# Performance work log

Measured on AMD Instinct MI355X. Metric: run time of the kernel, lower is better.

Reference implementation:

```python
import jax, jax.numpy as jnp
import numpy as np

COMMITMENT_COST = 0.25  # hardcoded in VQVAEModel (quantizer commitment_cost=0.25)


def setup_inputs() -> dict:
    key = jax.random.key(0)
    k1, k2 = jax.random.split(key)
    B, D, H, W = 128, 64, 32, 32
    K = 512
    inputs = jax.random.normal(k1, (B, D, H, W), dtype=jnp.float32)
    codebook = jax.random.normal(k2, (K, D), dtype=jnp.float32)  # nn.Embedding weight, normal_()
    return {"inputs": inputs, "codebook": codebook}


def reference(inputs, codebook):
    # VectorQuantizerEMA.forward in eval mode (no EMA buffer update).
    B, D, H, W = inputs.shape
    K = codebook.shape[0]
    # BCHW -> BHWC
    x = jnp.transpose(inputs, (0, 2, 3, 1))
    flat = x.reshape(-1, D)  # [N, D], N = B*H*W
    distances = (jnp.sum(flat * flat, axis=1, keepdims=True)
                 + jnp.sum(codebook * codebook, axis=1)
                 - 2.0 * flat @ codebook.T)
    # max_one_hot(-distances) == one-hot of argmin(distances)
    idx = jnp.argmin(distances, axis=1)  # [N]
    oh = jax.nn.one_hot(idx, K, dtype=flat.dtype)  # [N, K]
    # quantized = onehot @ codebook (detached) == gather, same math, cheaper
    quantized = jax.lax.stop_gradient(codebook[idx]).reshape(x.shape)  # [B,H,W,D]
    # commitment loss (quantized is detached under torch.no_grad)
    e_latent_loss = jnp.mean((quantized - x) ** 2)
    loss = COMMITMENT_COST * e_latent_loss
    # straight-through estimator
    q_st = x + jax.lax.stop_gradient(quantized - x)
    # perplexity of codebook usage
    avg_probs = jnp.mean(oh, axis=0)
    perplexity = jnp.exp(-jnp.sum(avg_probs * jnp.log(avg_probs + 1e-10)))
    # oh_encodings: rearrange '(b n) d -> b d n'
    oh_encodings = jnp.transpose(oh.reshape(B, H * W, K), (0, 2, 1))  # [B, K, N]
    quantized_out = jnp.transpose(q_st, (0, 3, 1, 2))  # back to BCHW
    return loss, quantized_out, perplexity, oh_encodings
```

## Files before the change

### kernel.cpp

```cpp
#include <hip/hip_runtime.h>
#include <hip/hip_bf16.h>
#include <float.h>

#define NTOT 131072

#define OFF_LOSS  0
#define OFF_QUANT 1
#define OFF_PERP  8388609
#define OFF_OH    8388610

#define FLAG_BIT (1 << 16)
#define TAU      1.5e-3f
#define MAGIC    0x5EEDF00D
#define WSTRIDE  516

typedef __attribute__((ext_vector_type(8))) short short8;
typedef __attribute__((ext_vector_type(4))) short short4v;
typedef __attribute__((ext_vector_type(4))) float f32x4;

__device__ inline unsigned short f2bf(float f) {
    unsigned u = __builtin_bit_cast(unsigned, f);
    unsigned r = (u + 0x7fffu + ((u >> 16) & 1u)) >> 16;
    return (unsigned short)r;
}
__device__ inline float bf2f(unsigned short h) {
    return __builtin_bit_cast(float, ((unsigned)h) << 16);
}

__global__ __launch_bounds__(1024)
void vq_fused(const float* __restrict__ x, const float* __restrict__ cb,
              int* __restrict__ wsi, float* __restrict__ out) {
    __shared__ short Ehi[512 * 64];
    __shared__ short Elo[512 * 64];
    __shared__ float en_s[512];
    __shared__ float dist_s[512];
    __shared__ int   idx_s[512];
    __shared__ int   hist_s[512];

    const int t = threadIdx.x, wg = blockIdx.x;
    const int w = t >> 6, lane = t & 63;
    const int c = lane & 15, g = lane >> 4;
    const int b0 = wg >> 1;
    const int sphalf = (wg & 1) << 9;
    float* qout = out + OFF_QUANT;
    float* oh   = out + OFF_OH;

    if (t < 512) hist_s[t] = 0;

    const float4* cb4 = (const float4*)cb;
#pragma unroll
    for (int i = 0; i < 8; ++i) {
        int e4 = i * 1024 + t;
        float4 v = cb4[e4];
        int k = e4 >> 4, q = e4 & 15;
        int base = (k << 6) + ((((q >> 1) ^ (k & 7)) << 3) + ((q & 1) << 2));
        float vv[4] = {v.x, v.y, v.z, v.w};
        short4v h4, l4;
#pragma unroll
        for (int e = 0; e < 4; ++e) {
            unsigned short h = f2bf(vv[e]);
            h4[e] = (short)h;
            l4[e] = (short)f2bf(vv[e] - bf2f(h));
        }
        *(short4v*)&Ehi[base] = h4;
        *(short4v*)&Elo[base] = l4;
    }
    if (t < 512) {
        const float4* r4 = cb4 + (t << 4);
        float s = 0.f;
#pragma unroll
        for (int j = 0; j < 16; ++j) {
            float4 vv = r4[j];
            s = fmaf(vv.x, vv.x, s); s = fmaf(vv.y, vv.y, s);
            s = fmaf(vv.z, vv.z, s); s = fmaf(vv.w, vv.w, s);
        }
        en_s[t] = s;
    }

    short8 bh[2][2], bl[2][2];
    float xn2[2] = {0.f, 0.f};
    const float* xb = x + (((size_t)b0) << 16) + sphalf + (w << 5) + c;
#pragma unroll
    for (int xt = 0; xt < 2; ++xt) {
#pragma unroll
        for (int ks = 0; ks < 2; ++ks) {
            short8 h8, l8;
#pragma unroll
            for (int e = 0; e < 8; ++e) {
                float xv = xb[(xt << 4) + ((size_t)((ks << 5) + (g << 3) + e) << 10)];
                unsigned short hh = f2bf(xv);
                h8[e] = (short)hh;
                l8[e] = (short)f2bf(xv - bf2f(hh));
                xn2[xt] = fmaf(xv, xv, xn2[xt]);
            }
            bh[xt][ks] = h8; bl[xt][ks] = l8;
        }
    }
    float xnorm[2];
#pragma unroll
    for (int xt = 0; xt < 2; ++xt) {
        float v = xn2[xt];
        v += __shfl_xor(v, 16);
        v += __shfl_xor(v, 32);
        xnorm[xt] = v;
    }
    __syncthreads();

    float v1[2] = {FLT_MAX, FLT_MAX}, v2[2] = {FLT_MAX, FLT_MAX};
    int   i1[2] = {0, 0},            i2v[2] = {0, 0};
    const int sw = c & 7;
    const short* ph = &Ehi[c << 6];
    const short* pl = &Elo[c << 6];
#pragma unroll 2
    for (int kt = 0; kt < 32; ++kt) {
        const short* rh = ph + (kt << 10);
        const short* rl = pl + (kt << 10);
        short8 ah0 = *(const short8*)(rh + ((g ^ sw) << 3));
        short8 ah1 = *(const short8*)(rh + (((g + 4) ^ sw) << 3));
        short8 al0 = *(const short8*)(rl + ((g ^ sw) << 3));
        short8 al1 = *(const short8*)(rl + (((g + 4) ^ sw) << 3));
        float4 en4 = *(const float4*)&en_s[(kt << 4) + (g << 2)];
        float en_[4] = {en4.x, en4.y, en4.z, en4.w};
#pragma unroll
        for (int xt = 0; xt < 2; ++xt) {
            f32x4 acc = {0.f, 0.f, 0.f, 0.f};
            acc = __builtin_amdgcn_mfma_f32_16x16x32_bf16(ah0, bh[xt][0], acc, 0, 0, 0);
            acc = __builtin_amdgcn_mfma_f32_16x16x32_bf16(ah1, bh[xt][1], acc, 0, 0, 0);
            acc = __builtin_amdgcn_mfma_f32_16x16x32_bf16(al0, bh[xt][0], acc, 0, 0, 0);
            acc = __builtin_amdgcn_mfma_f32_16x16x32_bf16(al1, bh[xt][1], acc, 0, 0, 0);
            acc = __builtin_amdgcn_mfma_f32_16x16x32_bf16(ah0, bl[xt][0], acc, 0, 0, 0);
            acc = __builtin_amdgcn_mfma_f32_16x16x32_bf16(ah1, bl[xt][1], acc, 0, 0, 0);
#pragma unroll
            for (int r = 0; r < 4; ++r) {
                float dd = fmaf(-2.0f, acc[r], en_[r]);
                int k = (kt << 4) + (g << 2) + r;
                bool lt1 = dd < v1[xt];
                bool lt2 = dd < v2[xt];
                v2[xt] = lt1 ? v1[xt] : (lt2 ? dd : v2[xt]);
                i2v[xt] = lt1 ? i1[xt] : (lt2 ? k : i2v[xt]);
                v1[xt] = lt1 ? dd : v1[xt];
                i1[xt] = lt1 ? k : i1[xt];
            }
        }
    }

#pragma unroll
    for (int xt = 0; xt < 2; ++xt) {
        float V1 = v1[xt], V2 = v2[xt]; int I1 = i1[xt], I2 = i2v[xt];
#pragma unroll
        for (int off = 16; off <= 32; off <<= 1) {
            float o1 = __shfl_xor(V1, off); int oi1 = __shfl_xor(I1, off);
            float o2 = __shfl_xor(V2, off); int oi2 = __shfl_xor(I2, off);
            if (o1 < V1 || (o1 == V1 && oi1 < I1)) {
                V2 = V1; I2 = I1; V1 = o1; I1 = oi1;
            } else if (o1 < V2 || (o1 == V2 && oi1 < I2)) { V2 = o1; I2 = oi1; }
            if (o2 < V2 || (o2 == V2 && oi2 < I2)) { V2 = o2; I2 = oi2; }
        }
        if (g == 0) {
            int r = (w << 5) + (xt << 4) + c;
            idx_s[r]  = I1 | ((V2 - V1 < TAU) ? FLAG_BIT : 0);
            dist_s[r] = xnorm[xt] + V1;
        }
    }
    __syncthreads();

    {
        int rowfull = (lane < 32) ? idx_s[(w << 5) + lane] : 0;
        unsigned long long m = __ballot((lane < 32) && (rowfull & FLAG_BIT));
        while (m) {
            int r = __ffsll((long long)m) - 1; m &= m - 1;
            int sp = sphalf + (w << 5) + r;
            float xd = x[(((size_t)b0) << 16) + (((size_t)lane) << 10) + sp];
            double bestd = 1e300; int besti = 0x7fffffff;
            for (int kk = 0; kk < 8; ++kk) {
                int k = (lane << 3) + kk;
                double s = 0.0;
#pragma unroll
                for (int d4 = 0; d4 < 16; ++d4) {
                    float4 e4 = cb4[(k << 4) + d4];
                    float x0 = __shfl(xd, d4 * 4 + 0);
                    float x1 = __shfl(xd, d4 * 4 + 1);
                    float x2 = __shfl(xd, d4 * 4 + 2);
                    float x3 = __shfl(xd, d4 * 4 + 3);
                    double f0 = (double)x0 - (double)e4.x; s = fma(f0, f0, s);
                    double f1 = (double)x1 - (double)e4.y; s = fma(f1, f1, s);
                    double f2 = (double)x2 - (double)e4.z; s = fma(f2, f2, s);
                    double f3 = (double)x3 - (double)e4.w; s = fma(f3, f3, s);
                }
                if (s < bestd || (s == bestd && k < besti)) { bestd = s; besti = k; }
            }
#pragma unroll
            for (int off = 32; off; off >>= 1) {
                double od = __shfl_xor(bestd, off);
                int    oi = __shfl_xor(besti, off);
                if (od < bestd || (od == bestd && oi < besti)) { bestd = od; besti = oi; }
            }
            if (lane == 0) {
                idx_s[(w << 5) + r]  = besti;
                dist_s[(w << 5) + r] = (float)bestd;
            }
        }
    }
    __syncthreads();

    if (t < 512) {
        int k = idx_s[t] & 511;
        idx_s[t] = k;
        atomicAdd(&hist_s[k], 1);
        float v = dist_s[t];
#pragma unroll
        for (int off = 1; off < 64; off <<= 1) v += __shfl_xor(v, off);
        if (lane == 0) en_s[w] = v;
    }
    __syncthreads();
    if (t < 512)
        __hip_atomic_store(&wsi[wg * WSTRIDE + t], hist_s[t],
                           __ATOMIC_RELAXED, __HIP_MEMORY_SCOPE_AGENT);
    if (t == 0) {
        float lsum = 0.f;
        for (int i = 0; i < 8; ++i) lsum += en_s[i];
        __hip_atomic_store(&wsi[wg * WSTRIDE + 512], __float_as_int(lsum),
                           __ATOMIC_RELAXED, __HIP_MEMORY_SCOPE_AGENT);
    }
    __syncthreads();
    if (t == 0)
        __hip_atomic_store(&wsi[wg * WSTRIDE + 513], MAGIC,
                           __ATOMIC_RELEASE, __HIP_MEMORY_SCOPE_AGENT);

    {
        float4 z4 = {0.f, 0.f, 0.f, 0.f};
        float2 z2 = {0.f, 0.f};
        float* base_wg = oh + (((size_t)b0) << 19) + sphalf;
        for (int j = 0; j < 32; ++j) {
            int k = w + (j << 4);
            float* cbase = base_wg + (((size_t)k) << 10);
            *(float4*)(cbase + 2 + (lane << 2)) = z4;
            if (lane < 63)
                *(float4*)(cbase + 2 + ((64 + lane) << 2)) = z4;
            else {
                *(float2*)(cbase)       = z2;
                *(float2*)(cbase + 510) = z2;
            }
        }
    }
    __syncthreads();

    if (t < 512) {
        int k = idx_s[t];
        oh[(((size_t)b0) << 19) + (((size_t)k) << 10) + sphalf + t] = 1.0f;
    }

    {
        float* qbase = qout + (((size_t)b0) << 16) + sphalf;
#pragma unroll
        for (int j = 0; j < 4; ++j) {
            int d = (w << 2) + j;
            const int ch = d >> 3, dj = d & 7;
            float* rb = qbase + (((size_t)d) << 10);
#pragma unroll
            for (int rnd = 0; rnd < 2; ++rnd) {
                int m = (rnd << 6) + lane;
                if (m < 127) {
                    int s0 = 3 + (m << 2);
                    float vv[4];
#pragma unroll
                    for (int e = 0; e < 4; ++e) {
                        int k = idx_s[s0 + e];
                        int a = (k << 6) + (((ch ^ (k & 7)) << 3) + dj);
                        vv[e] = bf2f((unsigned short)Ehi[a]) + bf2f((unsigned short)Elo[a]);
                    }
                    float4 v4 = {vv[0], vv[1], vv[2], vv[3]};
                    *(float4*)(rb + s0) = v4;
                } else if (rnd == 1) {
                    int k0 = idx_s[0], k1 = idx_s[1], k2 = idx_s[2], k5 = idx_s[511];
                    int a0 = (k0 << 6) + (((ch ^ (k0 & 7)) << 3) + dj);
                    int a1 = (k1 << 6) + (((ch ^ (k1 & 7)) << 3) + dj);
                    int a2 = (k2 << 6) + (((ch ^ (k2 & 7)) << 3) + dj);
                    int a5 = (k5 << 6) + (((ch ^ (k5 & 7)) << 3) + dj);
                    rb[0] = bf2f((unsigned short)Ehi[a0]) + bf2f((unsigned short)Elo[a0]);
                    float2 e2 = { bf2f((unsigned short)Ehi[a1]) + bf2f((unsigned short)Elo[a1]),
                                  bf2f((unsigned short)Ehi[a2]) + bf2f((unsigned short)Elo[a2]) };
                    *(float2*)(rb + 1) = e2;
                    rb[511] = bf2f((unsigned short)Ehi[a5]) + bf2f((unsigned short)Elo[a5]);
                }
            }
        }
    }

    if (wg == 0) {
        if (t < 256) {
            while (__hip_atomic_load(&wsi[t * WSTRIDE + 513],
                                     __ATOMIC_ACQUIRE, __HIP_MEMORY_SCOPE_AGENT) != MAGIC)
                __builtin_amdgcn_s_sleep(2);
        }
        __syncthreads();
        float plog = 0.f, lpart = 0.f;
        if (t < 512) {
            int s = 0;
            for (int wgi = 0; wgi < 256; ++wgi)
                s += __hip_atomic_load(&wsi[wgi * WSTRIDE + t],
                                       __ATOMIC_RELAXED, __HIP_MEMORY_SCOPE_AGENT);
            float p = (float)s * (1.f / (float)NTOT);
            plog = p * logf(p + 1e-10f);
        }
        if (t < 256)
            lpart = __int_as_float(__hip_atomic_load(&wsi[t * WSTRIDE + 512],
                                       __ATOMIC_RELAXED, __HIP_MEMORY_SCOPE_AGENT));
#pragma unroll
        for (int off = 1; off < 64; off <<= 1) {
            plog  += __shfl_xor(plog, off);
            lpart += __shfl_xor(lpart, off);
        }
        __syncthreads();
        if (lane == 0 && w < 8) en_s[w] = plog;
        if (lane == 0 && w < 4) dist_s[w] = lpart;
        __syncthreads();
        if (t == 0) {
            float ps = 0.f; for (int i = 0; i < 8; ++i) ps += en_s[i];
            float ls = 0.f; for (int i = 0; i < 4; ++i) ls += dist_s[i];
            out[OFF_PERP] = expf(-ps);
            out[OFF_LOSS] = 0.25f * ls / ((float)NTOT * 64.0f);
        }
    }
}

extern "C" void kernel_launch(void* const* d_in, const int* in_sizes, int n_in,
                              void* d_out, int out_size, void* d_ws, size_t ws_size,
                              hipStream_t stream) {
    const float* x  = (const float*)d_in[0];
    const float* cb = (const float*)d_in[1];
    vq_fused<<<256, 1024, 0, stream>>>(x, cb, (int*)d_ws, (float*)d_out);
}
```

Measured before the change: 417.6 us.

## Specialize waves: half compute argmin while other half zero one-hot output

Splits the 16 waves into two roles. Eight waves load inputs and run the MFMA distance/argmin over 64 rows each. The other eight waves convert the codebook into LDS during setup, then write the large zero fill of the one-hot output while the compute waves run. This hides the memory-bound zeroing behind the MFMA work and drops one barrier. In exchange, the compute waves carry twice the rows, so register pressure rises, and the codebook staging now runs on half the threads.

```diff
diff --git a/kernel.cpp b/kernel.cpp
--- a/kernel.cpp
+++ b/kernel.cpp
@@ -48,156 +48,176 @@
     if (t < 512) hist_s[t] = 0;
 
     const float4* cb4 = (const float4*)cb;
-#pragma unroll
-    for (int i = 0; i < 8; ++i) {
-        int e4 = i * 1024 + t;
-        float4 v = cb4[e4];
-        int k = e4 >> 4, q = e4 & 15;
-        int base = (k << 6) + ((((q >> 1) ^ (k & 7)) << 3) + ((q & 1) << 2));
-        float vv[4] = {v.x, v.y, v.z, v.w};
-        short4v h4, l4;
-#pragma unroll
-        for (int e = 0; e < 4; ++e) {
-            unsigned short h = f2bf(vv[e]);
-            h4[e] = (short)h;
-            l4[e] = (short)f2bf(vv[e] - bf2f(h));
-        }
-        *(short4v*)&Ehi[base] = h4;
-        *(short4v*)&Elo[base] = l4;
-    }
-    if (t < 512) {
-        const float4* r4 = cb4 + (t << 4);
-        float s = 0.f;
-#pragma unroll
-        for (int j = 0; j < 16; ++j) {
-            float4 vv = r4[j];
-            s = fmaf(vv.x, vv.x, s); s = fmaf(vv.y, vv.y, s);
-            s = fmaf(vv.z, vv.z, s); s = fmaf(vv.w, vv.w, s);
-        }
-        en_s[t] = s;
-    }
-
-    short8 bh[2][2], bl[2][2];
-    float xn2[2] = {0.f, 0.f};
-    const float* xb = x + (((size_t)b0) << 16) + sphalf + (w << 5) + c;
-#pragma unroll
-    for (int xt = 0; xt < 2; ++xt) {
-#pragma unroll
-        for (int ks = 0; ks < 2; ++ks) {
-            short8 h8, l8;
-#pragma unroll
-            for (int e = 0; e < 8; ++e) {
-                float xv = xb[(xt << 4) + ((size_t)((ks << 5) + (g << 3) + e) << 10)];
-                unsigned short hh = f2bf(xv);
-                h8[e] = (short)hh;
-                l8[e] = (short)f2bf(xv - bf2f(hh));
-                xn2[xt] = fmaf(xv, xv, xn2[xt]);
-            }
-            bh[xt][ks] = h8; bl[xt][ks] = l8;
-        }
-    }
-    float xnorm[2];
-#pragma unroll
-    for (int xt = 0; xt < 2; ++xt) {
-        float v = xn2[xt];
-        v += __shfl_xor(v, 16);
-        v += __shfl_xor(v, 32);
-        xnorm[xt] = v;
+
+    short8 bh[4][2], bl[4][2];
+    float xnorm[4];
+
+    if (w >= 8) {
+        int j = w - 8;
+#pragma unroll
+        for (int i = 0; i < 16; ++i) {
+            int e4 = (j << 6) + lane + (i << 9);
+            float4 v = cb4[e4];
+            int k = e4 >> 4, q = e4 & 15;
+            int base = (k << 6) + ((((q >> 1) ^ (k & 7)) << 3) + ((q & 1) << 2));
+            float vv[4] = {v.x, v.y, v.z, v.w};
+            short4v h4, l4;
+#pragma unroll
+            for (int e = 0; e < 4; ++e) {
+                unsigned short h = f2bf(vv[e]);
+                h4[e] = (short)h;
+                l4[e] = (short)f2bf(vv[e] - bf2f(h));
+            }
+            *(short4v*)&Ehi[base] = h4;
+            *(short4v*)&Elo[base] = l4;
+        }
+        {
+            int i = t - 512;
+            const float4* r4 = cb4 + (i << 4);
+            float s = 0.f;
+#pragma unroll
+            for (int jj = 0; jj < 16; ++jj) {
+                float4 vv = r4[jj];
+                s = fmaf(vv.x, vv.x, s); s = fmaf(vv.y, vv.y, s);
+                s = fmaf(vv.z, vv.z, s); s = fmaf(vv.w, vv.w, s);
+            }
+            en_s[i] = s;
+        }
+    } else {
+        const float* xb = x + (((size_t)b0) << 16) + sphalf + (w << 6) + c;
+#pragma unroll
+        for (int xt = 0; xt < 4; ++xt) {
+            float xn2 = 0.f;
+#pragma unroll
+            for (int ks = 0; ks < 2; ++ks) {
+                short8 h8, l8;
+#pragma unroll
+                for (int e = 0; e < 8; ++e) {
+                    float xv = xb[(xt << 4) + ((size_t)((ks << 5) + (g << 3) + e) << 10)];
+                    unsigned short hh = f2bf(xv);
+                    h8[e] = (short)hh;
+                    l8[e] = (short)f2bf(xv - bf2f(hh));
+                    xn2 = fmaf(xv, xv, xn2);
+                }
+                bh[xt][ks] = h8; bl[xt][ks] = l8;
+            }
+            xn2 += __shfl_xor(xn2, 16);
+            xn2 += __shfl_xor(xn2, 32);
+            xnorm[xt] = xn2;
+        }
     }
     __syncthreads();
 
-    float v1[2] = {FLT_MAX, FLT_MAX}, v2[2] = {FLT_MAX, FLT_MAX};
-    int   i1[2] = {0, 0},            i2v[2] = {0, 0};
-    const int sw = c & 7;
-    const short* ph = &Ehi[c << 6];
-    const short* pl = &Elo[c << 6];
-#pragma unroll 2
-    for (int kt = 0; kt < 32; ++kt) {
-        const short* rh = ph + (kt << 10);
-        const short* rl = pl + (kt << 10);
-        short8 ah0 = *(const short8*)(rh + ((g ^ sw) << 3));
-        short8 ah1 = *(const short8*)(rh + (((g + 4) ^ sw) << 3));
-        short8 al0 = *(const short8*)(rl + ((g ^ sw) << 3));
-        short8 al1 = *(const short8*)(rl + (((g + 4) ^ sw) << 3));
-        float4 en4 = *(const float4*)&en_s[(kt << 4) + (g << 2)];
-        float en_[4] = {en4.x, en4.y, en4.z, en4.w};
-#pragma unroll
-        for (int xt = 0; xt < 2; ++xt) {
-            f32x4 acc = {0.f, 0.f, 0.f, 0.f};
-            acc = __builtin_amdgcn_mfma_f32_16x16x32_bf16(ah0, bh[xt][0], acc, 0, 0, 0);
-            acc = __builtin_amdgcn_mfma_f32_16x16x32_bf16(ah1, bh[xt][1], acc, 0, 0, 0);
-            acc = __builtin_amdgcn_mfma_f32_16x16x32_bf16(al0, bh[xt][0], acc, 0, 0, 0);
-            acc = __builtin_amdgcn_mfma_f32_16x16x32_bf16(al1, bh[xt][1], acc, 0, 0, 0);
-            acc = __builtin_amdgcn_mfma_f32_16x16x32_bf16(ah0, bl[xt][0], acc, 0, 0, 0);
-            acc = __builtin_amdgcn_mfma_f32_16x16x32_bf16(ah1, bl[xt][1], acc, 0, 0, 0);
-#pragma unroll
-            for (int r = 0; r < 4; ++r) {
-                float dd = fmaf(-2.0f, acc[r], en_[r]);
-                int k = (kt << 4) + (g << 2) + r;
-                bool lt1 = dd < v1[xt];
-                bool lt2 = dd < v2[xt];
-                v2[xt] = lt1 ? v1[xt] : (lt2 ? dd : v2[xt]);
-                i2v[xt] = lt1 ? i1[xt] : (lt2 ? k : i2v[xt]);
-                v1[xt] = lt1 ? dd : v1[xt];
-                i1[xt] = lt1 ? k : i1[xt];
-            }
-        }
-    }
-
-#pragma unroll
-    for (int xt = 0; xt < 2; ++xt) {
-        float V1 = v1[xt], V2 = v2[xt]; int I1 = i1[xt], I2 = i2v[xt];
-#pragma unroll
-        for (int off = 16; off <= 32; off <<= 1) {
-            float o1 = __shfl_xor(V1, off); int oi1 = __shfl_xor(I1, off);
-            float o2 = __shfl_xor(V2, off); int oi2 = __shfl_xor(I2, off);
-            if (o1 < V1 || (o1 == V1 && oi1 < I1)) {
-                V2 = V1; I2 = I1; V1 = o1; I1 = oi1;
-            } else if (o1 < V2 || (o1 == V2 && oi1 < I2)) { V2 = o1; I2 = oi1; }
-            if (o2 < V2 || (o2 == V2 && oi2 < I2)) { V2 = o2; I2 = oi2; }
-        }
-        if (g == 0) {
-            int r = (w << 5) + (xt << 4) + c;
-            idx_s[r]  = I1 | ((V2 - V1 < TAU) ? FLAG_BIT : 0);
-            dist_s[r] = xnorm[xt] + V1;
-        }
-    }
-    __syncthreads();
-
-    {
-        int rowfull = (lane < 32) ? idx_s[(w << 5) + lane] : 0;
-        unsigned long long m = __ballot((lane < 32) && (rowfull & FLAG_BIT));
-        while (m) {
-            int r = __ffsll((long long)m) - 1; m &= m - 1;
-            int sp = sphalf + (w << 5) + r;
-            float xd = x[(((size_t)b0) << 16) + (((size_t)lane) << 10) + sp];
-            double bestd = 1e300; int besti = 0x7fffffff;
-            for (int kk = 0; kk < 8; ++kk) {
-                int k = (lane << 3) + kk;
-                double s = 0.0;
-#pragma unroll
-                for (int d4 = 0; d4 < 16; ++d4) {
-                    float4 e4 = cb4[(k << 4) + d4];
-                    float x0 = __shfl(xd, d4 * 4 + 0);
-                    float x1 = __shfl(xd, d4 * 4 + 1);
-                    float x2 = __shfl(xd, d4 * 4 + 2);
-                    float x3 = __shfl(xd, d4 * 4 + 3);
-                    double f0 = (double)x0 - (double)e4.x; s = fma(f0, f0, s);
-                    double f1 = (double)x1 - (double)e4.y; s = fma(f1, f1, s);
-                    double f2 = (double)x2 - (double)e4.z; s = fma(f2, f2, s);
-                    double f3 = (double)x3 - (double)e4.w; s = fma(f3, f3, s);
-                }
-                if (s < bestd || (s == bestd && k < besti)) { bestd = s; besti = k; }
-            }
-#pragma unroll
-            for (int off = 32; off; off >>= 1) {
-                double od = __shfl_xor(bestd, off);
-                int    oi = __shfl_xor(besti, off);
-                if (od < bestd || (od == bestd && oi < besti)) { bestd = od; besti = oi; }
-            }
-            if (lane == 0) {
-                idx_s[(w << 5) + r]  = besti;
-                dist_s[(w << 5) + r] = (float)bestd;
+    if (w < 8) {
+        float v1[4] = {FLT_MAX, FLT_MAX, FLT_MAX, FLT_MAX};
+        float v2[4] = {FLT_MAX, FLT_MAX, FLT_MAX, FLT_MAX};
+        int   i1[4] = {0, 0, 0, 0}, i2v[4] = {0, 0, 0, 0};
+        const int sw = c & 7;
+        const short* ph = &Ehi[c << 6];
+        const short* pl = &Elo[c << 6];
+        for (int kt = 0; kt < 32; ++kt) {
+            const short* rh = ph + (kt << 10);
+            const short* rl = pl + (kt << 10);
+            short8 ah0 = *(const short8*)(rh + ((g ^ sw) << 3));
+            short8 ah1 = *(const short8*)(rh + (((g + 4) ^ sw) << 3));
+            short8 al0 = *(const short8*)(rl + ((g ^ sw) << 3));
+            short8 al1 = *(const short8*)(rl + (((g + 4) ^ sw) << 3));
+            float4 en4 = *(const float4*)&en_s[(kt << 4) + (g << 2)];
+            float en_[4] = {en4.x, en4.y, en4.z, en4.w};
+#pragma unroll
+            for (int xt = 0; xt < 4; ++xt) {
+                f32x4 acc = {0.f, 0.f, 0.f, 0.f};
+                acc = __builtin_amdgcn_mfma_f32_16x16x32_bf16(ah0, bh[xt][0], acc, 0, 0, 0);
+                acc = __builtin_amdgcn_mfma_f32_16x16x32_bf16(ah1, bh[xt][1], acc, 0, 0, 0);
+                acc = __builtin_amdgcn_mfma_f32_16x16x32_bf16(al0, bh[xt][0], acc, 0, 0, 0);
+                acc = __builtin_amdgcn_mfma_f32_16x16x32_bf16(al1, bh[xt][1], acc, 0, 0, 0);
+                acc = __builtin_amdgcn_mfma_f32_16x16x32_bf16(ah0, bl[xt][0], acc, 0, 0, 0);
+                acc = __builtin_amdgcn_mfma_f32_16x16x32_bf16(ah1, bl[xt][1], acc, 0, 0, 0);
+#pragma unroll
+                for (int r = 0; r < 4; ++r) {
+                    float dd = fmaf(-2.0f, acc[r], en_[r]);
+                    int k = (kt << 4) + (g << 2) + r;
+                    bool lt1 = dd < v1[xt];
+                    bool lt2 = dd < v2[xt];
+                    v2[xt] = lt1 ? v1[xt] : (lt2 ? dd : v2[xt]);
+                    i2v[xt] = lt1 ? i1[xt] : (lt2 ? k : i2v[xt]);
+                    v1[xt] = lt1 ? dd : v1[xt];
+                    i1[xt] = lt1 ? k : i1[xt];
+                }
+            }
+        }
+
+#pragma unroll
+        for (int xt = 0; xt < 4; ++xt) {
+            float V1 = v1[xt], V2 = v2[xt]; int I1 = i1[xt], I2 = i2v[xt];
+#pragma unroll
+            for (int off = 16; off <= 32; off <<= 1) {
+                float o1 = __shfl_xor(V1, off); int oi1 = __shfl_xor(I1, off);
+                float o2 = __shfl_xor(V2, off); int oi2 = __shfl_xor(I2, off);
+                if (o1 < V1 || (o1 == V1 && oi1 < I1)) {
+                    V2 = V1; I2 = I1; V1 = o1; I1 = oi1;
+                } else if (o1 < V2 || (o1 == V2 && oi1 < I2)) { V2 = o1; I2 = oi1; }
+                if (o2 < V2 || (o2 == V2 && oi2 < I2)) { V2 = o2; I2 = oi2; }
+            }
+            if (g == 0) {
+                int r = (w << 6) + (xt << 4) + c;
+                idx_s[r]  = I1 | ((V2 - V1 < TAU) ? FLAG_BIT : 0);
+                dist_s[r] = xnorm[xt] + V1;
+            }
+        }
+
+        for (int half = 0; half < 2; ++half) {
+            int rbase = (w << 6) + (half << 5);
+            int rowfull = (lane < 32) ? idx_s[rbase + lane] : 0;
+            unsigned long long m = __ballot((lane < 32) && (rowfull & FLAG_BIT));
+            while (m) {
+                int r = __ffsll((long long)m) - 1; m &= m - 1;
+                int sp = sphalf + rbase + r;
+                float xd = x[(((size_t)b0) << 16) + (((size_t)lane) << 10) + sp];
+                double bestd = 1e300; int besti = 0x7fffffff;
+                for (int kk = 0; kk < 8; ++kk) {
+                    int k = (lane << 3) + kk;
+                    double s = 0.0;
+#pragma unroll
+                    for (int d4 = 0; d4 < 16; ++d4) {
+                        float4 e4 = cb4[(k << 4) + d4];
+                        float x0 = __shfl(xd, d4 * 4 + 0);
+                        float x1 = __shfl(xd, d4 * 4 + 1);
+                        float x2 = __shfl(xd, d4 * 4 + 2);
+                        float x3 = __shfl(xd, d4 * 4 + 3);
+                        double f0 = (double)x0 - (double)e4.x; s = fma(f0, f0, s);
+                        double f1 = (double)x1 - (double)e4.y; s = fma(f1, f1, s);
+                        double f2 = (double)x2 - (double)e4.z; s = fma(f2, f2, s);
+                        double f3 = (double)x3 - (double)e4.w; s = fma(f3, f3, s);
+                    }
+                    if (s < bestd || (s == bestd && k < besti)) { bestd = s; besti = k; }
+                }
+#pragma unroll
+                for (int off = 32; off; off >>= 1) {
+                    double od = __shfl_xor(bestd, off);
+                    int    oi = __shfl_xor(besti, off);
+                    if (od < bestd || (od == bestd && oi < besti)) { bestd = od; besti = oi; }
+                }
+                if (lane == 0) {
+                    idx_s[rbase + r]  = besti;
+                    dist_s[rbase + r] = (float)bestd;
+                }
+            }
+        }
+    } else {
+        int j = w - 8;
+        float4 z4 = {0.f, 0.f, 0.f, 0.f};
+        float2 z2 = {0.f, 0.f};
+        float* base_wg = oh + (((size_t)b0) << 19) + sphalf;
+        for (int it = 0; it < 64; ++it) {
+            int k = j + (it << 3);
+            float* cbase = base_wg + (((size_t)k) << 10);
+            *(float4*)(cbase + 2 + (lane << 2)) = z4;
+            if (lane < 63)
+                *(float4*)(cbase + 2 + ((64 + lane) << 2)) = z4;
+            else {
+                *(float2*)(cbase)       = z2;
+                *(float2*)(cbase + 510) = z2;
             }
         }
     }
@@ -226,24 +246,6 @@
     if (t == 0)
         __hip_atomic_store(&wsi[wg * WSTRIDE + 513], MAGIC,
                            __ATOMIC_RELEASE, __HIP_MEMORY_SCOPE_AGENT);
-
-    {
-        float4 z4 = {0.f, 0.f, 0.f, 0.f};
-        float2 z2 = {0.f, 0.f};
-        float* base_wg = oh + (((size_t)b0) << 19) + sphalf;
-        for (int j = 0; j < 32; ++j) {
-            int k = w + (j << 4);
-            float* cbase = base_wg + (((size_t)k) << 10);
-            *(float4*)(cbase + 2 + (lane << 2)) = z4;
-            if (lane < 63)
-                *(float4*)(cbase + 2 + ((64 + lane) << 2)) = z4;
-            else {
-                *(float2*)(cbase)       = z2;
-                *(float2*)(cbase + 510) = z2;
-            }
-        }
-    }
-    __syncthreads();
 
     if (t < 512) {
         int k = idx_s[t];
```

After: 413.2 us. About the same (-1.1%).

## Split codebook prep kernel, halve block size and LDS, use global atomics for stats

Applied to the files above, without the earlier changes.

Adds a small prep kernel that precomputes the bf16 low-part codebook into workspace and zeroes the global counters. The main kernel now runs 512 blocks of 512 threads, keeps only the high part in LDS and reads the low part from global/L2. The per-block histogram/loss handoff through a polled workspace array is replaced by global atomicAdds and a done counter. The quantized output is gathered straight from the fp32 codebook. The smaller LDS footprint is meant to raise occupancy, at the cost of an extra launch and global-memory loads in the inner MFMA loop.

```diff
diff --git a/kernel.cpp b/kernel.cpp
--- a/kernel.cpp
+++ b/kernel.cpp
@@ -11,8 +11,8 @@
 
 #define FLAG_BIT (1 << 16)
 #define TAU      1.5e-3f
-#define MAGIC    0x5EEDF00D
-#define WSTRIDE  516
+
+#define W_ELO 640
 
 typedef __attribute__((ext_vector_type(8))) short short8;
 typedef __attribute__((ext_vector_type(4))) short short4v;
@@ -27,45 +27,65 @@
     return __builtin_bit_cast(float, ((unsigned)h) << 16);
 }
 
-__global__ __launch_bounds__(1024)
-void vq_fused(const float* __restrict__ x, const float* __restrict__ cb,
-              int* __restrict__ wsi, float* __restrict__ out) {
+__global__ __launch_bounds__(512)
+void vq_prep(const float* __restrict__ cb, int* __restrict__ wsi) {
+    int tid = blockIdx.x * 512 + threadIdx.x;
+    if (tid < 514) wsi[tid] = 0;
+    short* elo = (short*)(wsi + W_ELO);
+    int row = tid >> 1, half = tid & 1;
+    const float4* cb4 = (const float4*)cb;
+#pragma unroll
+    for (int j = 0; j < 8; ++j) {
+        float4 v = cb4[(row << 4) + (half << 3) + j];
+        float vv[4] = {v.x, v.y, v.z, v.w};
+        short4v l4;
+#pragma unroll
+        for (int e = 0; e < 4; ++e) {
+            unsigned short h = f2bf(vv[e]);
+            l4[e] = (short)f2bf(vv[e] - bf2f(h));
+        }
+        *(short4v*)(elo + (row << 6) + (half << 5) + (j << 2)) = l4;
+    }
+}
+
+__global__ __launch_bounds__(512, 4)
+void vq_main(const float* __restrict__ x, const float* __restrict__ cb,
+             int* __restrict__ wsi, float* __restrict__ out) {
     __shared__ short Ehi[512 * 64];
-    __shared__ short Elo[512 * 64];
     __shared__ float en_s[512];
-    __shared__ float dist_s[512];
-    __shared__ int   idx_s[512];
+    __shared__ float dist_s[256];
+    __shared__ int   idx_s[256];
     __shared__ int   hist_s[512];
+    __shared__ float lpart_s[4];
 
     const int t = threadIdx.x, wg = blockIdx.x;
     const int w = t >> 6, lane = t & 63;
     const int c = lane & 15, g = lane >> 4;
-    const int b0 = wg >> 1;
-    const int sphalf = (wg & 1) << 9;
+    const int b = wg >> 2;
+    const int sp0 = (wg & 3) << 8;
     float* qout = out + OFF_QUANT;
     float* oh   = out + OFF_OH;
+    float* loss_g = (float*)wsi;
+    int*   done_g = wsi + 1;
+    int*   cnt_g  = wsi + 2;
+    const short* elo_t = (const short*)(wsi + W_ELO);
 
     if (t < 512) hist_s[t] = 0;
 
     const float4* cb4 = (const float4*)cb;
 #pragma unroll
-    for (int i = 0; i < 8; ++i) {
-        int e4 = i * 1024 + t;
+    for (int i = 0; i < 16; ++i) {
+        int e4 = i * 512 + t;
         float4 v = cb4[e4];
-        int k = e4 >> 4, q = e4 & 15;
-        int base = (k << 6) + ((((q >> 1) ^ (k & 7)) << 3) + ((q & 1) << 2));
+        int k = e4 >> 4, q4 = e4 & 15;
+        int base = (k << 6) + ((((q4 >> 1) ^ (k & 7)) << 3) + ((q4 & 1) << 2));
         float vv[4] = {v.x, v.y, v.z, v.w};
-        short4v h4, l4;
-#pragma unroll
-        for (int e = 0; e < 4; ++e) {
-            unsigned short h = f2bf(vv[e]);
-            h4[e] = (short)h;
-            l4[e] = (short)f2bf(vv[e] - bf2f(h));
-        }
+        short4v h4;
+#pragma unroll
+        for (int e = 0; e < 4; ++e) h4[e] = (short)f2bf(vv[e]);
         *(short4v*)&Ehi[base] = h4;
-        *(short4v*)&Elo[base] = l4;
-    }
-    if (t < 512) {
+    }
+    {
         const float4* r4 = cb4 + (t << 4);
         float s = 0.f;
 #pragma unroll
@@ -78,10 +98,11 @@
     }
 
     short8 bh[2][2], bl[2][2];
-    float xn2[2] = {0.f, 0.f};
-    const float* xb = x + (((size_t)b0) << 16) + sphalf + (w << 5) + c;
+    float xnorm[2];
+    const float* xb = x + (((size_t)b) << 16) + sp0 + (w << 5) + c;
 #pragma unroll
     for (int xt = 0; xt < 2; ++xt) {
+        float xn2 = 0.f;
 #pragma unroll
         for (int ks = 0; ks < 2; ++ks) {
             short8 h8, l8;
@@ -91,18 +112,13 @@
                 unsigned short hh = f2bf(xv);
                 h8[e] = (short)hh;
                 l8[e] = (short)f2bf(xv - bf2f(hh));
-                xn2[xt] = fmaf(xv, xv, xn2[xt]);
+                xn2 = fmaf(xv, xv, xn2);
             }
             bh[xt][ks] = h8; bl[xt][ks] = l8;
         }
-    }
-    float xnorm[2];
-#pragma unroll
-    for (int xt = 0; xt < 2; ++xt) {
-        float v = xn2[xt];
-        v += __shfl_xor(v, 16);
-        v += __shfl_xor(v, 32);
-        xnorm[xt] = v;
+        xn2 += __shfl_xor(xn2, 16);
+        xn2 += __shfl_xor(xn2, 32);
+        xnorm[xt] = xn2;
     }
     __syncthreads();
 
@@ -110,15 +126,13 @@
     int   i1[2] = {0, 0},            i2v[2] = {0, 0};
     const int sw = c & 7;
     const short* ph = &Ehi[c << 6];
-    const short* pl = &Elo[c << 6];
-#pragma unroll 2
+    const short* pel = elo_t + (c << 6) + (g << 3);
     for (int kt = 0; kt < 32; ++kt) {
         const short* rh = ph + (kt << 10);
-        const short* rl = pl + (kt << 10);
         short8 ah0 = *(const short8*)(rh + ((g ^ sw) << 3));
         short8 ah1 = *(const short8*)(rh + (((g + 4) ^ sw) << 3));
-        short8 al0 = *(const short8*)(rl + ((g ^ sw) << 3));
-        short8 al1 = *(const short8*)(rl + (((g + 4) ^ sw) << 3));
+        short8 al0 = *(const short8*)(pel + (kt << 10));
+        short8 al1 = *(const short8*)(pel + (kt << 10) + 32);
         float4 en4 = *(const float4*)&en_s[(kt << 4) + (g << 2)];
         float en_[4] = {en4.x, en4.y, en4.z, en4.w};
 #pragma unroll
@@ -162,15 +176,15 @@
             dist_s[r] = xnorm[xt] + V1;
         }
     }
-    __syncthreads();
 
     {
-        int rowfull = (lane < 32) ? idx_s[(w << 5) + lane] : 0;
+        int rbase = w << 5;
+        int rowfull = (lane < 32) ? idx_s[rbase + lane] : 0;
         unsigned long long m = __ballot((lane < 32) && (rowfull & FLAG_BIT));
         while (m) {
             int r = __ffsll((long long)m) - 1; m &= m - 1;
-            int sp = sphalf + (w << 5) + r;
-            float xd = x[(((size_t)b0) << 16) + (((size_t)lane) << 10) + sp];
+            int sp = sp0 + rbase + r;
+            float xd = x[(((size_t)b) << 16) + (((size_t)lane) << 10) + sp];
             double bestd = 1e300; int besti = 0x7fffffff;
             for (int kk = 0; kk < 8; ++kk) {
                 int k = (lane << 3) + kk;
@@ -196,129 +210,89 @@
                 if (od < bestd || (od == bestd && oi < besti)) { bestd = od; besti = oi; }
             }
             if (lane == 0) {
-                idx_s[(w << 5) + r]  = besti;
-                dist_s[(w << 5) + r] = (float)bestd;
+                idx_s[rbase + r]  = besti;
+                dist_s[rbase + r] = (float)bestd;
             }
         }
     }
     __syncthreads();
 
-    if (t < 512) {
+    if (t < 256) {
         int k = idx_s[t] & 511;
         idx_s[t] = k;
         atomicAdd(&hist_s[k], 1);
-        float v = dist_s[t];
-#pragma unroll
-        for (int off = 1; off < 64; off <<= 1) v += __shfl_xor(v, off);
-        if (lane == 0) en_s[w] = v;
+        float lv = dist_s[t];
+#pragma unroll
+        for (int off = 1; off < 64; off <<= 1) lv += __shfl_xor(lv, off);
+        if (lane == 0) lpart_s[w] = lv;
     }
     __syncthreads();
-    if (t < 512)
-        __hip_atomic_store(&wsi[wg * WSTRIDE + t], hist_s[t],
-                           __ATOMIC_RELAXED, __HIP_MEMORY_SCOPE_AGENT);
+    if (t < 512 && hist_s[t]) atomicAdd(&cnt_g[t], hist_s[t]);
     if (t == 0) {
-        float lsum = 0.f;
-        for (int i = 0; i < 8; ++i) lsum += en_s[i];
-        __hip_atomic_store(&wsi[wg * WSTRIDE + 512], __float_as_int(lsum),
-                           __ATOMIC_RELAXED, __HIP_MEMORY_SCOPE_AGENT);
-    }
-    __syncthreads();
-    if (t == 0)
-        __hip_atomic_store(&wsi[wg * WSTRIDE + 513], MAGIC,
-                           __ATOMIC_RELEASE, __HIP_MEMORY_SCOPE_AGENT);
+        atomicAdd(loss_g, lpart_s[0] + lpart_s[1] + lpart_s[2] + lpart_s[3]);
+        __hip_atomic_fetch_add(done_g, 1, __ATOMIC_RELEASE, __HIP_MEMORY_SCOPE_AGENT);
+    }
 
     {
         float4 z4 = {0.f, 0.f, 0.f, 0.f};
         float2 z2 = {0.f, 0.f};
-        float* base_wg = oh + (((size_t)b0) << 19) + sphalf;
-        for (int j = 0; j < 32; ++j) {
-            int k = w + (j << 4);
+        float* base_wg = oh + (((size_t)b) << 19) + sp0;
+        for (int it = 0; it < 64; ++it) {
+            int k = (it << 3) + w;
             float* cbase = base_wg + (((size_t)k) << 10);
-            *(float4*)(cbase + 2 + (lane << 2)) = z4;
             if (lane < 63)
-                *(float4*)(cbase + 2 + ((64 + lane) << 2)) = z4;
+                *(float4*)(cbase + 2 + (lane << 2)) = z4;
             else {
                 *(float2*)(cbase)       = z2;
-                *(float2*)(cbase + 510) = z2;
+                *(float2*)(cbase + 254) = z2;
             }
         }
     }
     __syncthreads();
 
-    if (t < 512) {
+    if (t < 256) {
         int k = idx_s[t];
-        oh[(((size_t)b0) << 19) + (((size_t)k) << 10) + sphalf + t] = 1.0f;
+        oh[(((size_t)b) << 19) + (((size_t)k) << 10) + sp0 + t] = 1.0f;
     }
 
     {
-        float* qbase = qout + (((size_t)b0) << 16) + sphalf;
-#pragma unroll
-        for (int j = 0; j < 4; ++j) {
-            int d = (w << 2) + j;
-            const int ch = d >> 3, dj = d & 7;
-            float* rb = qbase + (((size_t)d) << 10);
-#pragma unroll
-            for (int rnd = 0; rnd < 2; ++rnd) {
-                int m = (rnd << 6) + lane;
-                if (m < 127) {
-                    int s0 = 3 + (m << 2);
-                    float vv[4];
-#pragma unroll
-                    for (int e = 0; e < 4; ++e) {
-                        int k = idx_s[s0 + e];
-                        int a = (k << 6) + (((ch ^ (k & 7)) << 3) + dj);
-                        vv[e] = bf2f((unsigned short)Ehi[a]) + bf2f((unsigned short)Elo[a]);
-                    }
-                    float4 v4 = {vv[0], vv[1], vv[2], vv[3]};
-                    *(float4*)(rb + s0) = v4;
-                } else if (rnd == 1) {
-                    int k0 = idx_s[0], k1 = idx_s[1], k2 = idx_s[2], k5 = idx_s[511];
-                    int a0 = (k0 << 6) + (((ch ^ (k0 & 7)) << 3) + dj);
-                    int a1 = (k1 << 6) + (((ch ^ (k1 & 7)) << 3) + dj);
-                    int a2 = (k2 << 6) + (((ch ^ (k2 & 7)) << 3) + dj);
-                    int a5 = (k5 << 6) + (((ch ^ (k5 & 7)) << 3) + dj);
-                    rb[0] = bf2f((unsigned short)Ehi[a0]) + bf2f((unsigned short)Elo[a0]);
-                    float2 e2 = { bf2f((unsigned short)Ehi[a1]) + bf2f((unsigned short)Elo[a1]),
-                                  bf2f((unsigned short)Ehi[a2]) + bf2f((unsigned short)Elo[a2]) };
-                    *(float2*)(rb + 1) = e2;
-                    rb[511] = bf2f((unsigned short)Ehi[a5]) + bf2f((unsigned short)Elo[a5]);
-                }
-            }
+        int r = t & 255, half = t >> 8;
+        int k = idx_s[r];
+        float* qb = qout + (((size_t)b) << 16) + sp0 + r;
+#pragma unroll
+        for (int j = 0; j < 8; ++j) {
+            float4 v = cb4[(k << 4) + (half << 3) + j];
+            int d0 = (half << 5) + (j << 2);
+            qb[((size_t)(d0 + 0)) << 10] = v.x;
+            qb[((size_t)(d0 + 1)) << 10] = v.y;
+            qb[((size_t)(d0 + 2)) << 10] = v.z;
+            qb[((size_t)(d0 + 3)) << 10] = v.w;
         }
     }
 
     if (wg == 0) {
-        if (t < 256) {
-            while (__hip_atomic_load(&wsi[t * WSTRIDE + 513],
-                                     __ATOMIC_ACQUIRE, __HIP_MEMORY_SCOPE_AGENT) != MAGIC)
+        if (t == 0) {
+            while (__hip_atomic_load(done_g, __ATOMIC_ACQUIRE,
+                                     __HIP_MEMORY_SCOPE_AGENT) != 512)
                 __builtin_amdgcn_s_sleep(2);
         }
         __syncthreads();
-        float plog = 0.f, lpart = 0.f;
-        if (t < 512) {
-            int s = 0;
-            for (int wgi = 0; wgi < 256; ++wgi)
-                s += __hip_atomic_load(&wsi[wgi * WSTRIDE + t],
-                                       __ATOMIC_RELAXED, __HIP_MEMORY_SCOPE_AGENT);
+        float plog = 0.f;
+        {
+            int s = __hip_atomic_load(&cnt_g[t], __ATOMIC_RELAXED,
+                                      __HIP_MEMORY_SCOPE_AGENT);
             float p = (float)s * (1.f / (float)NTOT);
             plog = p * logf(p + 1e-10f);
         }
-        if (t < 256)
-            lpart = __int_as_float(__hip_atomic_load(&wsi[t * WSTRIDE + 512],
-                                       __ATOMIC_RELAXED, __HIP_MEMORY_SCOPE_AGENT));
-#pragma unroll
-        for (int off = 1; off < 64; off <<= 1) {
-            plog  += __shfl_xor(plog, off);
-            lpart += __shfl_xor(lpart, off);
-        }
-        __syncthreads();
-        if (lane == 0 && w < 8) en_s[w] = plog;
-        if (lane == 0 && w < 4) dist_s[w] = lpart;
+#pragma unroll
+        for (int off = 1; off < 64; off <<= 1) plog += __shfl_xor(plog, off);
+        if (lane == 0) en_s[w] = plog;
         __syncthreads();
         if (t == 0) {
-            float ps = 0.f; for (int i = 0; i < 8; ++i) ps += en_s[i];
-            float ls = 0.f; for (int i = 0; i < 4; ++i) ls += dist_s[i];
+            float ps = 0.f;
+            for (int i = 0; i < 8; ++i) ps += en_s[i];
             out[OFF_PERP] = expf(-ps);
+            float ls = *((volatile float*)loss_g);
             out[OFF_LOSS] = 0.25f * ls / ((float)NTOT * 64.0f);
         }
     }
@@ -329,5 +303,6 @@
                               hipStream_t stream) {
     const float* x  = (const float*)d_in[0];
     const float* cb = (const float*)d_in[1];
-    vq_fused<<<256, 1024, 0, stream>>>(x, cb, (int*)d_ws, (float*)d_out);
-}
+    vq_prep<<<2,   512, 0, stream>>>(cb, (int*)d_ws);
+    vq_main<<<512, 512, 0, stream>>>(x, cb, (int*)d_ws, (float*)d_out);
+}
```

After: 445.5 us. 1.07x slower.
